# Kernel optimization log

Measured on AMD Instinct MI355X. Metric: run time of the kernel, lower is better.

The kernel has to match this reference:

```python
import jax, jax.numpy as jnp
import numpy as np

LOGIT_SCALE_MAX = float(np.log(1.0 / 0.01))  # log(100)
EPS = 1e-12  # F.normalize eps


def setup_inputs() -> dict:
    key = jax.random.key(0)
    ks = jax.random.split(key, 4)
    L, N, C, H = 1024, 8, 1024, 16
    x = jax.random.normal(ks[0], (L, N, C), dtype=jnp.float32)
    w_in = jax.random.normal(ks[1], (3 * C, C), dtype=jnp.float32) * 0.02
    b_in = jnp.zeros((3 * C,), dtype=jnp.float32)
    logit_scale = jnp.full((H, 1, 1), float(np.log(10.0)), dtype=jnp.float32)
    head_scale = jnp.ones((H, 1, 1), dtype=jnp.float32)
    w_out = jax.random.normal(ks[2], (C, C), dtype=jnp.float32) * 0.02
    b_out = jnp.zeros((C,), dtype=jnp.float32)
    return {"x": x, "w_in": w_in, "b_in": b_in, "logit_scale": logit_scale,
            "head_scale": head_scale, "w_out": w_out, "b_out": b_out}


def _l2norm(t):
    # matches F.normalize(t, dim=-1): t / max(||t||, eps)
    n = jnp.sqrt(jnp.sum(t * t, axis=-1, keepdims=True))
    return t / jnp.maximum(n, EPS)


def reference(x, w_in, b_in, logit_scale, head_scale, w_out, b_out):
    L, N, C = x.shape
    H = logit_scale.shape[0]
    D = C // H
    qkv = x @ w_in.T + b_in                      # (L, N, 3C)
    q, k, v = jnp.split(qkv, 3, axis=-1)         # each (L, N, C)

    def to_heads(t):                             # (L, N, C) -> (N*H, L, D)
        return t.reshape(L, N * H, D).transpose(1, 0, 2)

    q, k, v = to_heads(q), to_heads(k), to_heads(v)
    # cosine-similarity logits with clamped learned per-head scale
    attn = jnp.einsum('bld,bmd->blm', _l2norm(q), _l2norm(k))  # (N*H, L, L)
    ls = jnp.exp(jnp.minimum(logit_scale, LOGIT_SCALE_MAX))    # (H,1,1)
    attn = (attn.reshape(N, H, L, L) * ls).reshape(N * H, L, L)
    attn = jax.nn.softmax(attn, axis=-1)
    out = jnp.einsum('blm,bmd->bld', attn, v)    # (N*H, L, D)
    # per-head scaling (intended math of the head_scale branch)
    out = (out.reshape(N, H, L, D) * head_scale).reshape(N * H, L, D)
    out = out.transpose(1, 0, 2).reshape(L, N, C)
    out = out @ w_out.T + b_out
    return out, attn
```

## Files before the change

kernel.cpp:

```cpp
#include <hip/hip_runtime.h>
#include <hip/hip_fp16.h>
#include <cstdint>

typedef _Float16 f16;
typedef _Float16 f16x4 __attribute__((ext_vector_type(4)));
typedef _Float16 f16x8 __attribute__((ext_vector_type(8)));
typedef float f32x4 __attribute__((ext_vector_type(4)));

#define MFMA16(a, b, c) __builtin_amdgcn_mfma_f32_16x16x32_f16(a, b, c, 0, 0, 0)

constexpr int Lq = 1024, Nb = 8, Cc = 1024, Hh = 16, Dd = 64;
constexpr int Mrows = Lq * Nb;
constexpr float LOG100 = 4.6051701859880913680f;
constexpr float LOG2E = 1.4426950408889634f;

typedef const __attribute__((address_space(1))) unsigned int* gu32p;
typedef __attribute__((address_space(3))) unsigned int* lu32p;
__device__ __forceinline__ void gl_lds16(const void* g, void* l) {
  __builtin_amdgcn_global_load_lds((gu32p)g, (lu32p)l, 16, 0, 0);
}

__global__ __launch_bounds__(256) void k_cvt(const float* __restrict__ in,
                                             f16* __restrict__ out, int n8) {
  int i = blockIdx.x * blockDim.x + threadIdx.x;
  if (i >= n8) return;
  const float4* p = (const float4*)in + (size_t)i * 2;
  float4 a = p[0], b = p[1];
  f16x8 o = {(f16)a.x, (f16)a.y, (f16)a.z, (f16)a.w,
             (f16)b.x, (f16)b.y, (f16)b.z, (f16)b.w};
  *((f16x8*)out + i) = o;
}

template <typename OutT>
__global__ __launch_bounds__(256) void k_gemm(const f16* __restrict__ A,
                                              const f16* __restrict__ B,
                                              const float* __restrict__ bias,
                                              OutT* __restrict__ Co,
                                              int Np, int Kd) {
  __shared__ f16 Ash[128 * 64];
  __shared__ f16 Bsh[128 * 64];
  const int tid = threadIdx.x, lane = tid & 63, wid = tid >> 6;
  const int m0 = blockIdx.y * 128, n0 = blockIdx.x * 128;
  const int wy = wid >> 1, wx = wid & 1;
  const int rq = lane & 15, kq = lane >> 4;
  f32x4 acc[4][4] = {};
  const int nkt = Kd >> 6;
  for (int kt = 0; kt < nkt; ++kt) {
    __syncthreads();
    for (int iss = 0; iss < 4; ++iss) {
      int cbase = (iss * 4 + wid) * 64;
      int c = cbase + lane;
      int row = ((c >> 7) << 4) + (c & 15);
      int col = kt * 64 + ((c >> 6) & 1) * 32 + ((c >> 4) & 3) * 8;
      gl_lds16(A + (size_t)(m0 + row) * Kd + col, (char*)Ash + cbase * 16);
      gl_lds16(B + (size_t)(n0 + row) * Kd + col, (char*)Bsh + cbase * 16);
    }
    __syncthreads();
    for (int ks = 0; ks < 2; ++ks) {
      f16x8 af[4], bf[4];
      for (int t = 0; t < 4; ++t)
        af[t] = *(const f16x8*)((const char*)Ash + ((((wy * 4 + t) * 2 + ks) * 64 + lane) * 16));
      for (int u = 0; u < 4; ++u)
        bf[u] = *(const f16x8*)((const char*)Bsh + ((((wx * 4 + u) * 2 + ks) * 64 + lane) * 16));
      for (int t = 0; t < 4; ++t)
        for (int u = 0; u < 4; ++u)
          acc[t][u] = MFMA16(af[t], bf[u], acc[t][u]);
    }
  }
  for (int t = 0; t < 4; ++t) {
    int row = m0 + wy * 64 + t * 16 + 4 * kq;
    for (int u = 0; u < 4; ++u) {
      int col = n0 + wx * 64 + u * 16 + rq;
      float bv = bias[col];
      for (int rr = 0; rr < 4; ++rr) {
        float v = acc[t][u][rr] + bv;
        Co[(size_t)(row + rr) * Np + col] = (OutT)v;
      }
    }
  }
}

__global__ __launch_bounds__(256) void k_norm(const f16* __restrict__ qkv,
                                              f16* __restrict__ qhat,
                                              f16* __restrict__ khat,
                                              f16* __restrict__ vTt) {
  __shared__ f16 vt[64][72];
  const int blk = blockIdx.x;
  const int b = blk >> 4, lc = blk & 15;
  const int h = b & 15, n = b >> 4;
  const int tid = threadIdx.x;
  const int g4 = tid >> 2, sub = tid & 3;
  const int lrow = lc * 64 + g4;
  const size_t srow = ((size_t)lrow * Nb + n) * 3072;
  for (int qk = 0; qk < 2; ++qk) {
    const f16* p = qkv + srow + qk * 1024 + h * 64 + sub * 16;
    f16x8 a = *(const f16x8*)p;
    f16x8 c2 = *(const f16x8*)(p + 8);
    float ss = 0.f;
    for (int e = 0; e < 8; ++e) { float x = (float)a[e]; ss += x * x; }
    for (int e = 0; e < 8; ++e) { float x = (float)c2[e]; ss += x * x; }
    ss += __shfl_xor(ss, 1);
    ss += __shfl_xor(ss, 2);
    float sc = 1.f / fmaxf(sqrtf(ss), 1e-12f);
    f16x8 oa, ob;
    for (int e = 0; e < 8; ++e) oa[e] = (f16)((float)a[e] * sc);
    for (int e = 0; e < 8; ++e) ob[e] = (f16)((float)c2[e] * sc);
    f16* dst = (qk ? khat : qhat) + ((size_t)b * Lq + lrow) * Dd + sub * 16;
    *(f16x8*)dst = oa;
    *(f16x8*)(dst + 8) = ob;
  }
  {
    const f16* p = qkv + srow + 2048 + h * 64 + sub * 16;
    f16x8 a = *(const f16x8*)p;
    f16x8 c2 = *(const f16x8*)(p + 8);
    for (int e = 0; e < 8; ++e) vt[g4][sub * 16 + e] = a[e];
    for (int e = 0; e < 8; ++e) vt[g4][sub * 16 + 8 + e] = c2[e];
  }
  __syncthreads();
  {
    const int d = g4;
    f16x8 oa, ob;
    for (int e = 0; e < 8; ++e) oa[e] = vt[sub * 16 + e][d];
    for (int e = 0; e < 8; ++e) ob[e] = vt[sub * 16 + 8 + e][d];
    f16* dst = vTt + ((size_t)b * Dd + d) * Lq + lc * 64 + sub * 16;
    *(f16x8*)dst = oa;
    *(f16x8*)(dst + 8) = ob;
  }
}

__global__ __launch_bounds__(256) void k_attn(const f16* __restrict__ qhat,
                                              const f16* __restrict__ khat,
                                              const f16* __restrict__ vTt,
                                              const float* __restrict__ lsc,
                                              const float* __restrict__ hsc,
                                              float* __restrict__ attn,
                                              f16* __restrict__ Ows) {
  __shared__ f16 Kst[4096];
  __shared__ f16 Vst[4096];
  __shared__ f16 Pst[4][1024];
  const int blk = blockIdx.x;
  const int b = blk >> 4, qc = blk & 15;
  const int h = b & 15, n = b >> 4;
  const int tid = threadIdx.x, lane = tid & 63, w = tid >> 6;
  const int rq = lane & 15, kq = lane >> 4;
  const int ib = qc * 64 + w * 16;
  const float ls = __expf(fminf(lsc[h], LOG100));
  const float hs = hsc[h];
  const float c1 = ls * LOG2E, c0 = -c1;
  const f16* qb = qhat + ((size_t)b * Lq + ib) * Dd;
  f16x8 qf0 = *(const f16x8*)(qb + (size_t)rq * Dd + kq * 8);
  f16x8 qf1 = *(const f16x8*)(qb + (size_t)rq * Dd + 32 + kq * 8);
  const f16* kb = khat + (size_t)b * Lq * Dd;
  const f16* vb = vTt + (size_t)b * Dd * Lq;
  f16* Pw = Pst[w];

  float lsum = 0.f;
  f32x4 Oa[4] = {};
  for (int kt = 0; kt < 16; ++kt) {
    const int j0 = kt * 64;
    __syncthreads();
    for (int iss = 0; iss < 2; ++iss) {
      int cbase = (iss * 4 + w) * 64;
      int c = cbase + lane;
      int rq_ = c & 15, kq_ = (c >> 4) & 3, h_ = (c >> 6) & 1, u_ = c >> 7;
      gl_lds16(kb + (size_t)(j0 + u_ * 16 + rq_) * Dd + h_ * 32 + kq_ * 8,
               (char*)Kst + cbase * 16);
      gl_lds16(vb + (size_t)(u_ * 16 + rq_) * Lq + j0 + h_ * 32 + kq_ * 8,
               (char*)Vst + cbase * 16);
    }
    __syncthreads();
    f32x4 s[4];
    for (int u = 0; u < 4; ++u) {
      f16x8 k0 = *(const f16x8*)(Kst + (u * 128 + lane) * 8);
      f16x8 k1 = *(const f16x8*)(Kst + (u * 128 + 64 + lane) * 8);
      f32x4 a = {0.f, 0.f, 0.f, 0.f};
      a = MFMA16(k0, qf0, a);
      a = MFMA16(k1, qf1, a);
      s[u] = a;
    }
    for (int u = 0; u < 4; ++u) {
      f16x4 t4;
      for (int rr = 0; rr < 4; ++rr) {
        float e = exp2f(fmaf(s[u][rr], c1, c0));
        lsum += e;
        t4[rr] = (f16)e;
      }
      int cw = (u >> 1) * 64 + ((2 * u + (kq >> 1)) & 3) * 16 + rq;
      *(f16x4*)(Pw + cw * 8 + (kq & 1) * 4) = t4;
    }
    f16x8 pa0 = *(const f16x8*)(Pw + (kq * 16 + rq) * 8);
    f16x8 pa1 = *(const f16x8*)(Pw + (64 + kq * 16 + rq) * 8);
    for (int t = 0; t < 4; ++t) {
      f16x8 v0 = *(const f16x8*)(Vst + (t * 128 + lane) * 8);
      f16x8 v1 = *(const f16x8*)(Vst + (t * 128 + 64 + lane) * 8);
      Oa[t] = MFMA16(pa0, v0, Oa[t]);
      Oa[t] = MFMA16(pa1, v1, Oa[t]);
    }
  }
  lsum += __shfl_xor(lsum, 16);
  lsum += __shfl_xor(lsum, 32);
  const float invl = 1.f / lsum;

  float* ab = attn + (size_t)b * Lq * Lq + (size_t)(ib + rq) * Lq;
  for (int kt = 0; kt < 16; ++kt) {
    const int j0 = kt * 64;
    __syncthreads();
    {
      int cbase = w * 64 + ((lane >> 5) ? 1024 : 0);
    }
    for (int iss = 0; iss < 2; ++iss) {
      int cbase = (iss * 4 + w) * 64;
      int c = cbase + lane;
      int rq_ = c & 15, kq_ = (c >> 4) & 3, h_ = (c >> 6) & 1, u_ = c >> 7;
      gl_lds16(kb + (size_t)(j0 + u_ * 16 + rq_) * Dd + h_ * 32 + kq_ * 8,
               (char*)Kst + cbase * 16);
    }
    __syncthreads();
    f32x4 s[4];
    for (int u = 0; u < 4; ++u) {
      f16x8 k0 = *(const f16x8*)(Kst + (u * 128 + lane) * 8);
      f16x8 k1 = *(const f16x8*)(Kst + (u * 128 + 64 + lane) * 8);
      f32x4 a = {0.f, 0.f, 0.f, 0.f};
      a = MFMA16(k0, qf0, a);
      a = MFMA16(k1, qf1, a);
      s[u] = a;
    }
    for (int u = 0; u < 4; ++u) {
      f32x4 p;
      for (int rr = 0; rr < 4; ++rr)
        p[rr] = exp2f(fmaf(s[u][rr], c1, c0)) * invl;
      *(f32x4*)(ab + j0 + u * 16 + 4 * kq) = p;
    }
  }

  float invlO[4];
  for (int rr = 0; rr < 4; ++rr) invlO[rr] = __shfl(invl, 4 * kq + rr);
  for (int t = 0; t < 4; ++t) {
    for (int rr = 0; rr < 4; ++rr) {
      int iseq = ib + 4 * kq + rr;
      int d = t * 16 + rq;
      Ows[((size_t)iseq * Nb + n) * Cc + h * Dd + d] = (f16)(Oa[t][rr] * invlO[rr] * hs);
    }
  }
}

extern "C" void kernel_launch(void* const* d_in, const int* in_sizes, int n_in,
                              void* d_out, int out_size, void* d_ws, size_t ws_size,
                              hipStream_t stream) {
  const float* x     = (const float*)d_in[0];
  const float* w_in  = (const float*)d_in[1];
  const float* b_in  = (const float*)d_in[2];
  const float* lsc   = (const float*)d_in[3];
  const float* hsc   = (const float*)d_in[4];
  const float* w_out = (const float*)d_in[5];
  const float* b_out = (const float*)d_in[6];
  float* out  = (float*)d_out;
  float* attn = out + (size_t)Mrows * Cc;

  char* ws = (char*)d_ws;
  f16* xh   = (f16*)(ws + 0);
  f16* wh   = (f16*)(ws + 16777216);
  f16* wo   = (f16*)(ws + 23068672);
  f16* qkv  = (f16*)(ws + 25165824);
  f16* qhat = (f16*)(ws + 75497472);
  f16* khat = (f16*)(ws + 92274688);
  f16* vTt  = (f16*)(ws + 109051904);
  f16* Ows  = (f16*)(ws + 125829120);
  if (ws_size < 142606336ull) return;

  k_cvt<<<(Mrows * Cc / 8 + 255) / 256, 256, 0, stream>>>(x, xh, Mrows * Cc / 8);
  k_cvt<<<(3072 * 1024 / 8 + 255) / 256, 256, 0, stream>>>(w_in, wh, 3072 * 1024 / 8);
  k_cvt<<<(1024 * 1024 / 8 + 255) / 256, 256, 0, stream>>>(w_out, wo, 1024 * 1024 / 8);
  k_gemm<f16><<<dim3(24, 64), 256, 0, stream>>>(xh, wh, b_in, qkv, 3072, 1024);
  k_norm<<<2048, 256, 0, stream>>>(qkv, qhat, khat, vTt);
  k_attn<<<2048, 256, 0, stream>>>(qhat, khat, vTt, lsc, hsc, attn, Ows);
  k_gemm<float><<<dim3(8, 64), 256, 0, stream>>>(Ows, wo, b_out, out, 1024, 1024);
}
```

Measured before the change: 864.5 us.

## Split attention into PV pass and separate softmax-probability writer kernel

The fused attention kernel is split in two. One kernel computes the row sums and the PV output and stores the inverse row sum to a buffer that reuses the xh workspace. A second kernel recomputes QK^T and writes the normalized fp32 attention matrix. Block indexing is also changed so that blocks sharing a query chunk across heads are scheduled together. The aim is to separate the bandwidth-heavy 512MB attention write from the compute-heavy pass so each kernel can keep more waves resident, at the cost of an extra launch and a small round trip for the row sums.

```diff
diff --git a/kernel.cpp b/kernel.cpp
--- a/kernel.cpp
+++ b/kernel.cpp
@@ -128,18 +128,18 @@
   }
 }
 
-__global__ __launch_bounds__(256) void k_attn(const f16* __restrict__ qhat,
-                                              const f16* __restrict__ khat,
-                                              const f16* __restrict__ vTt,
-                                              const float* __restrict__ lsc,
-                                              const float* __restrict__ hsc,
-                                              float* __restrict__ attn,
-                                              f16* __restrict__ Ows) {
+__global__ __launch_bounds__(256) void k_attn_pv(const f16* __restrict__ qhat,
+                                                 const f16* __restrict__ khat,
+                                                 const f16* __restrict__ vTt,
+                                                 const float* __restrict__ lsc,
+                                                 const float* __restrict__ hsc,
+                                                 float* __restrict__ invlb,
+                                                 f16* __restrict__ Ows) {
   __shared__ f16 Kst[4096];
   __shared__ f16 Vst[4096];
   __shared__ f16 Pst[4][1024];
   const int blk = blockIdx.x;
-  const int b = blk >> 4, qc = blk & 15;
+  const int b = blk & 127, qc = blk >> 7;
   const int h = b & 15, n = b >> 4;
   const int tid = threadIdx.x, lane = tid & 63, w = tid >> 6;
   const int rq = lane & 15, kq = lane >> 4;
@@ -200,38 +200,7 @@
   lsum += __shfl_xor(lsum, 16);
   lsum += __shfl_xor(lsum, 32);
   const float invl = 1.f / lsum;
-
-  float* ab = attn + (size_t)b * Lq * Lq + (size_t)(ib + rq) * Lq;
-  for (int kt = 0; kt < 16; ++kt) {
-    const int j0 = kt * 64;
-    __syncthreads();
-    {
-      int cbase = w * 64 + ((lane >> 5) ? 1024 : 0);
-    }
-    for (int iss = 0; iss < 2; ++iss) {
-      int cbase = (iss * 4 + w) * 64;
-      int c = cbase + lane;
-      int rq_ = c & 15, kq_ = (c >> 4) & 3, h_ = (c >> 6) & 1, u_ = c >> 7;
-      gl_lds16(kb + (size_t)(j0 + u_ * 16 + rq_) * Dd + h_ * 32 + kq_ * 8,
-               (char*)Kst + cbase * 16);
-    }
-    __syncthreads();
-    f32x4 s[4];
-    for (int u = 0; u < 4; ++u) {
-      f16x8 k0 = *(const f16x8*)(Kst + (u * 128 + lane) * 8);
-      f16x8 k1 = *(const f16x8*)(Kst + (u * 128 + 64 + lane) * 8);
-      f32x4 a = {0.f, 0.f, 0.f, 0.f};
-      a = MFMA16(k0, qf0, a);
-      a = MFMA16(k1, qf1, a);
-      s[u] = a;
-    }
-    for (int u = 0; u < 4; ++u) {
-      f32x4 p;
-      for (int rr = 0; rr < 4; ++rr)
-        p[rr] = exp2f(fmaf(s[u][rr], c1, c0)) * invl;
-      *(f32x4*)(ab + j0 + u * 16 + 4 * kq) = p;
-    }
-  }
+  if (kq == 0) invlb[b * Lq + ib + rq] = invl;
 
   float invlO[4];
   for (int rr = 0; rr < 4; ++rr) invlO[rr] = __shfl(invl, 4 * kq + rr);
@@ -240,6 +209,51 @@
       int iseq = ib + 4 * kq + rr;
       int d = t * 16 + rq;
       Ows[((size_t)iseq * Nb + n) * Cc + h * Dd + d] = (f16)(Oa[t][rr] * invlO[rr] * hs);
+    }
+  }
+}
+
+__global__ __launch_bounds__(256) void k_attn_sm(const f16* __restrict__ qhat,
+                                                 const f16* __restrict__ khat,
+                                                 const float* __restrict__ invlb,
+                                                 const float* __restrict__ lsc,
+                                                 float* __restrict__ attn) {
+  __shared__ f16 Kst[4096];
+  const int blk = blockIdx.x;
+  const int b = blk & 127, qc = blk >> 7;
+  const int h = b & 15;
+  const int tid = threadIdx.x, lane = tid & 63, w = tid >> 6;
+  const int rq = lane & 15, kq = lane >> 4;
+  const int ib = qc * 64 + w * 16;
+  const float ls = __expf(fminf(lsc[h], LOG100));
+  const float c1 = ls * LOG2E, c0 = -c1;
+  const f16* qb = qhat + ((size_t)b * Lq + ib) * Dd;
+  f16x8 qf0 = *(const f16x8*)(qb + (size_t)rq * Dd + kq * 8);
+  f16x8 qf1 = *(const f16x8*)(qb + (size_t)rq * Dd + 32 + kq * 8);
+  const f16* kb = khat + (size_t)b * Lq * Dd;
+  const float invl = invlb[b * Lq + ib + rq];
+  float* ab = attn + (size_t)b * Lq * Lq + (size_t)(ib + rq) * Lq;
+  for (int kt = 0; kt < 16; ++kt) {
+    const int j0 = kt * 64;
+    __syncthreads();
+    for (int iss = 0; iss < 2; ++iss) {
+      int cbase = (iss * 4 + w) * 64;
+      int c = cbase + lane;
+      int rq_ = c & 15, kq_ = (c >> 4) & 3, h_ = (c >> 6) & 1, u_ = c >> 7;
+      gl_lds16(kb + (size_t)(j0 + u_ * 16 + rq_) * Dd + h_ * 32 + kq_ * 8,
+               (char*)Kst + cbase * 16);
+    }
+    __syncthreads();
+    for (int u = 0; u < 4; ++u) {
+      f16x8 k0 = *(const f16x8*)(Kst + (u * 128 + lane) * 8);
+      f16x8 k1 = *(const f16x8*)(Kst + (u * 128 + 64 + lane) * 8);
+      f32x4 a = {0.f, 0.f, 0.f, 0.f};
+      a = MFMA16(k0, qf0, a);
+      a = MFMA16(k1, qf1, a);
+      f32x4 p;
+      for (int rr = 0; rr < 4; ++rr)
+        p[rr] = exp2f(fmaf(a[rr], c1, c0)) * invl;
+      *(f32x4*)(ab + j0 + u * 16 + 4 * kq) = p;
     }
   }
 }
@@ -266,6 +280,7 @@
   f16* khat = (f16*)(ws + 92274688);
   f16* vTt  = (f16*)(ws + 109051904);
   f16* Ows  = (f16*)(ws + 125829120);
+  float* invlb = (float*)xh;
   if (ws_size < 142606336ull) return;
 
   k_cvt<<<(Mrows * Cc / 8 + 255) / 256, 256, 0, stream>>>(x, xh, Mrows * Cc / 8);
@@ -273,6 +288,7 @@
   k_cvt<<<(1024 * 1024 / 8 + 255) / 256, 256, 0, stream>>>(w_out, wo, 1024 * 1024 / 8);
   k_gemm<f16><<<dim3(24, 64), 256, 0, stream>>>(xh, wh, b_in, qkv, 3072, 1024);
   k_norm<<<2048, 256, 0, stream>>>(qkv, qhat, khat, vTt);
-  k_attn<<<2048, 256, 0, stream>>>(qhat, khat, vTt, lsc, hsc, attn, Ows);
+  k_attn_pv<<<2048, 256, 0, stream>>>(qhat, khat, vTt, lsc, hsc, invlb, Ows);
+  k_attn_sm<<<2048, 256, 0, stream>>>(qhat, khat, invlb, lsc, attn);
   k_gemm<float><<<dim3(8, 64), 256, 0, stream>>>(Ows, wo, b_out, out, 1024, 1024);
 }
```

Measured after the change: 873.6 us. About the same (+1.1%).
